# Performance work log

Hardware: AMD Instinct MI355X
Metric: run time of the kernel (lower is better)

## Reference

```python
import jax, jax.numpy as jnp
import numpy as np

N_HEAD = 16
D_MODEL = 1024
D_K = D_MODEL // N_HEAD  # 64
LN_EPS = 1e-5


def setup_inputs() -> dict:
    key = jax.random.key(0)
    ks = jax.random.split(key, 12)
    B, L, D = 4, 2048, D_MODEL
    std_qkv = float(np.sqrt(2.0 / (D + D_K)))
    q = jax.random.normal(ks[0], (B, L, D), jnp.float32)
    k = jax.random.normal(ks[1], (B, L, D), jnp.float32)
    v = jax.random.normal(ks[2], (B, L, D), jnp.float32)
    Wq = jax.random.normal(ks[3], (D, D), jnp.float32) * std_qkv
    Wk = jax.random.normal(ks[4], (D, D), jnp.float32) * std_qkv
    Wv = jax.random.normal(ks[5], (D, D), jnp.float32) * std_qkv
    bq = jnp.zeros((D,), jnp.float32)
    bk = jnp.zeros((D,), jnp.float32)
    bv = jnp.zeros((D,), jnp.float32)
    # xavier normal for fc: std = sqrt(2/(fan_in+fan_out))
    Wo = jax.random.normal(ks[6], (D, D), jnp.float32) * float(np.sqrt(2.0 / (D + D)))
    bo = jnp.zeros((D,), jnp.float32)
    gamma = jnp.ones((D,), jnp.float32)
    beta = jnp.zeros((D,), jnp.float32)
    return {"q": q, "k": k, "v": v, "Wq": Wq, "bq": bq, "Wk": Wk, "bk": bk,
            "Wv": Wv, "bv": bv, "Wo": Wo, "bo": bo, "gamma": gamma, "beta": beta}


def _layer_norm(x, gamma, beta):
    mu = jnp.mean(x, axis=-1, keepdims=True)
    var = jnp.mean(jnp.square(x - mu), axis=-1, keepdims=True)
    return (x - mu) * jax.lax.rsqrt(var + LN_EPS) * gamma + beta


def reference(q, k, v, Wq, bq, Wk, bk, Wv, bv, Wo, bo, gamma, beta):
    B, Lq, D = q.shape
    Lk = k.shape[1]
    h, dk = N_HEAD, D_K
    residual = q
    # projections (torch Linear: x @ W.T + b), split heads -> (h, b, l, dk)
    qh = (q @ Wq.T + bq).reshape(B, Lq, h, dk).transpose(2, 0, 1, 3)
    kh = (k @ Wk.T + bk).reshape(B, Lk, h, dk).transpose(2, 0, 1, 3)
    vh = (v @ Wv.T + bv).reshape(B, Lk, h, dk).transpose(2, 0, 1, 3)
    temp = jnp.asarray(np.power(dk, 0.5), qh.dtype)
    scores = jnp.einsum('hbqd,hbkd->hbqk', qh, kh) / temp
    attn = jax.nn.softmax(scores, axis=-1)  # softmax over key dim (dim=2 of bmm view)
    out = jnp.einsum('hbqk,hbkd->hbqd', attn, vh)
    # (h,b,lq,dk) -> (b,lq,h*dk)
    out = out.transpose(1, 2, 0, 3).reshape(B, Lq, D)
    out = out @ Wo.T + bo  # dropout p=0.0 -> identity
    out = _layer_norm(out + residual, gamma, beta)
    attn_flat = attn.reshape(h * B, Lq, Lk)  # matches torch (n_head*sz_b, lq, lk)
    return out, attn_flat
```

## Files before the change

kernel.cpp:

```cpp
#include <hip/hip_runtime.h>
#include <stdint.h>

typedef short bf16x8 __attribute__((ext_vector_type(8)));
typedef float f32x4 __attribute__((ext_vector_type(4)));
typedef unsigned short us4 __attribute__((ext_vector_type(4)));
typedef unsigned short us8 __attribute__((ext_vector_type(8)));
typedef unsigned uint2v __attribute__((ext_vector_type(2)));

#define SCL 0.18033688011112042f

__device__ __forceinline__ unsigned short f2bf(float f) {
  union { float f; unsigned u; } v; v.f = f;
  unsigned r = v.u + 0x7fffu + ((v.u >> 16) & 1u);
  return (unsigned short)(r >> 16);
}

__device__ __forceinline__ unsigned cvtpk(float lo, float hi) {
  unsigned r;
  asm("v_cvt_pk_bf16_f32 %0, %1, %2" : "=v"(r) : "v"(lo), "v"(hi));
  return r;
}

__device__ __forceinline__ float bf2f(unsigned short h) {
  union { unsigned u; float f; } v; v.u = ((unsigned)h) << 16; return v.f;
}

#define GL2LDS(g, l) __builtin_amdgcn_global_load_lds( \
    (const __attribute__((address_space(1))) void*)(g), \
    (__attribute__((address_space(3))) void*)(l), 16, 0, 0)

__global__ __launch_bounds__(256) void convert_all(
    const float* __restrict__ q, const float* __restrict__ k, const float* __restrict__ v,
    const float* __restrict__ wq, const float* __restrict__ wk, const float* __restrict__ wv,
    const float* __restrict__ wo,
    unsigned short* __restrict__ qb, unsigned short* __restrict__ kb, unsigned short* __restrict__ vb,
    unsigned short* __restrict__ wqb, unsigned short* __restrict__ wkb, unsigned short* __restrict__ wvb,
    unsigned short* __restrict__ wob)
{
  const long NB = 8388608, NW = 1048576;
  long i = ((long)blockIdx.x * 256 + threadIdx.x) * 4;
  if (i >= 3*NB + 4*NW) return;
  const float* src; unsigned short* dst; long off;
  if (i < NB)              { src = q;  dst = qb;  off = i; }
  else if (i < 2*NB)       { src = k;  dst = kb;  off = i - NB; }
  else if (i < 3*NB)       { src = v;  dst = vb;  off = i - 2*NB; }
  else if (i < 3*NB+NW)    { src = wq; dst = wqb; off = i - 3*NB; }
  else if (i < 3*NB+2*NW)  { src = wk; dst = wkb; off = i - 3*NB - NW; }
  else if (i < 3*NB+3*NW)  { src = wv; dst = wvb; off = i - 3*NB - 2*NW; }
  else                     { src = wo; dst = wob; off = i - 3*NB - 3*NW; }
  float4 x = *(const float4*)(src + off);
  us4 o; o.x = f2bf(x.x); o.y = f2bf(x.y); o.z = f2bf(x.z); o.w = f2bf(x.w);
  *(us4*)(dst + off) = o;
}

__global__ __launch_bounds__(256, 2) void qkv_gemm(
    const unsigned short* __restrict__ qb, const unsigned short* __restrict__ kb,
    const unsigned short* __restrict__ vb,
    const unsigned short* __restrict__ wqb, const unsigned short* __restrict__ wkb,
    const unsigned short* __restrict__ wvb,
    const float* __restrict__ bq, const float* __restrict__ bk, const float* __restrict__ bv,
    unsigned short* __restrict__ qh, unsigned short* __restrict__ kh,
    unsigned short* __restrict__ vt)
{
  const int z = blockIdx.z;
  const unsigned short* X = (z == 0) ? qb : (z == 1) ? kb : vb;
  const unsigned short* W = (z == 0) ? wqb : (z == 1) ? wkb : wvb;
  const float* bias = (z == 0) ? bq : (z == 1) ? bk : bv;
  unsigned short* dqh = (z == 0) ? qh : kh;
  const float sc = (z == 0) ? SCL : 1.0f;

  const int flat = blockIdx.x + (blockIdx.y << 6);
  const int xcd = flat & 7, ii = flat >> 3;
  const int m0 = (xcd * 8 + (ii & 7)) * 128;
  const int n0 = (ii >> 3) * 128;

  const int tid = threadIdx.x, lane = tid & 63, w = tid >> 6;
  const int wr = w >> 1, wc = w & 1;
  const int lg = lane >> 4, ll = lane & 15;

  __shared__ __align__(16) unsigned short As[2 * 128 * 32];
  __shared__ __align__(16) unsigned short Bs[2 * 128 * 32];

  f32x4 acc[4][4] = {};

  const char* gA = (const char*)X + ((size_t)(m0 + w*32 + (lane >> 2)) * 1024) * 2 + (lane & 3) * 16;
  const char* gB = (const char*)W + ((size_t)(n0 + w*32 + (lane >> 2)) * 1024) * 2 + (lane & 3) * 16;

#define STAGE_G(buf) do { \
    char* lA_ = (char*)As + (buf)*8192 + w*2048; \
    char* lB_ = (char*)Bs + (buf)*8192 + w*2048; \
    GL2LDS(gA, lA_); GL2LDS(gA + 32768, lA_ + 1024); \
    GL2LDS(gB, lB_); GL2LDS(gB + 32768, lB_ + 1024); \
    gA += 64; gB += 64; } while (0)

  STAGE_G(0);
  __syncthreads();

  for (int k0 = 0; k0 < 1024; k0 += 32) {
    const int cur = (k0 >> 5) & 1;
    if (k0 < 992) STAGE_G(cur ^ 1);
    const unsigned short* Ac = As + cur * 4096;
    const unsigned short* Bc = Bs + cur * 4096;
    bf16x8 xa[4], wb[4];
    const int kc = lg * 8;
#pragma unroll
    for (int f = 0; f < 4; ++f) xa[f] = *(const bf16x8*)&Ac[(wr*64 + f*16 + ll)*32 + kc];
#pragma unroll
    for (int f = 0; f < 4; ++f) wb[f] = *(const bf16x8*)&Bc[(wc*64 + f*16 + ll)*32 + kc];
    if (z < 2) {
#pragma unroll
      for (int fn = 0; fn < 4; ++fn)
#pragma unroll
        for (int fm = 0; fm < 4; ++fm)
          acc[fn][fm] = __builtin_amdgcn_mfma_f32_16x16x32_bf16(wb[fn], xa[fm], acc[fn][fm], 0, 0, 0);
    } else {
#pragma unroll
      for (int fm = 0; fm < 4; ++fm)
#pragma unroll
        for (int fn = 0; fn < 4; ++fn)
          acc[fm][fn] = __builtin_amdgcn_mfma_f32_16x16x32_bf16(xa[fm], wb[fn], acc[fm][fn], 0, 0, 0);
    }
    __syncthreads();
  }

  if (z < 2) {
#pragma unroll
    for (int fn = 0; fn < 4; ++fn) {
      const int n_g = n0 + wc*64 + fn*16 + lg*4;
      const float4 b4 = *(const float4*)&bias[n_g];
      const int h = n_g >> 6, dkk = n_g & 63;
#pragma unroll
      for (int fm = 0; fm < 4; ++fm) {
        const int m_g = m0 + wr*64 + fm*16 + ll;
        const int b_ = m_g >> 11, l_ = m_g & 2047;
        us4 pk;
        pk.x = f2bf((acc[fn][fm][0] + b4.x) * sc);
        pk.y = f2bf((acc[fn][fm][1] + b4.y) * sc);
        pk.z = f2bf((acc[fn][fm][2] + b4.z) * sc);
        pk.w = f2bf((acc[fn][fm][3] + b4.w) * sc);
        *(us4*)&dqh[((size_t)(h*4 + b_) * 2048 + l_) * 64 + dkk] = pk;
      }
    }
  } else {
#pragma unroll
    for (int fn = 0; fn < 4; ++fn) {
      const int n_g = n0 + wc*64 + fn*16 + ll;
      const float bias_n = bias[n_g];
      const int h = n_g >> 6, dkk = n_g & 63;
#pragma unroll
      for (int fm = 0; fm < 4; ++fm) {
        const int mrow = m0 + wr*64 + fm*16 + lg*4;
        const int b_ = mrow >> 11, l_ = mrow & 2047;
        us4 pk;
        pk.x = f2bf(acc[fm][fn][0] + bias_n);
        pk.y = f2bf(acc[fm][fn][1] + bias_n);
        pk.z = f2bf(acc[fm][fn][2] + bias_n);
        pk.w = f2bf(acc[fm][fn][3] + bias_n);
        *(us4*)&vt[((size_t)(h*4 + b_) * 64 + dkk) * 2048 + l_] = pk;
      }
    }
  }
}

__global__ __launch_bounds__(256, 3) void attn_kernel(
    const unsigned short* __restrict__ qh, const unsigned short* __restrict__ kh,
    const unsigned short* __restrict__ vt, float* __restrict__ probs,
    unsigned short* __restrict__ attn_o)
{
  const int bid = blockIdx.x;
  const int xcd = bid & 7;
  const int idx = bid >> 3;
  const int hb  = xcd * 8 + (idx & 7);
  const int qt  = idx >> 3;

  const int tid = threadIdx.x, lane = tid & 63, w = tid >> 6;
  const int wr = w >> 1, wc = w & 1;
  const int lg = lane >> 4, ll = lane & 15;

  __shared__ __align__(16) char smem[38400];
  unsigned short* Pb = (unsigned short*)smem;
  float* rs   = (float*)(smem + 36864);
  float* invl = (float*)(smem + 37888);
  float* Ored = (float*)smem;

  const size_t slab = (size_t)hb << 17;

  bf16x8 qf[4][2];
#pragma unroll
  for (int fq = 0; fq < 4; ++fq)
#pragma unroll
    for (int dh = 0; dh < 2; ++dh)
      qf[fq][dh] = *(const bf16x8*)&qh[slab + (size_t)(qt*128 + wr*64 + fq*16 + ll)*64 + dh*32 + lg*8];

  const unsigned short* Kf = kh + slab + (size_t)(wc*32 + ll)*64 + lg*8;
  const unsigned short* Vf = vt + slab + (size_t)ll*2048 + wc*32 + lg*8;

  float rsum[4] = {0.f, 0.f, 0.f, 0.f};
  for (int kt = 0; kt < 32; ++kt) {
    bf16x8 ka[2][2];
#pragma unroll
    for (int fk = 0; fk < 2; ++fk)
#pragma unroll
      for (int dh = 0; dh < 2; ++dh)
        ka[fk][dh] = *(const bf16x8*)(Kf + kt*4096 + fk*1024 + dh*32);
    f32x4 s[2][4] = {};
    __builtin_amdgcn_s_setprio(1);
#pragma unroll
    for (int dh = 0; dh < 2; ++dh)
#pragma unroll
      for (int fk = 0; fk < 2; ++fk)
#pragma unroll
        for (int fq = 0; fq < 4; ++fq)
          s[fk][fq] = __builtin_amdgcn_mfma_f32_16x16x32_bf16(ka[fk][dh], qf[fq][dh], s[fk][fq], 0, 0, 0);
    __builtin_amdgcn_s_setprio(0);
#pragma unroll
    for (int fk = 0; fk < 2; ++fk)
#pragma unroll
      for (int fq = 0; fq < 4; ++fq)
#pragma unroll
        for (int r = 0; r < 4; ++r)
          rsum[fq] += exp2f(s[fk][fq][r]);
  }

#pragma unroll
  for (int fq = 0; fq < 4; ++fq) {
    float t = rsum[fq];
    t += __shfl_xor(t, 16);
    t += __shfl_xor(t, 32);
    rsum[fq] = t;
  }
  if (lg == 0) {
#pragma unroll
    for (int fq = 0; fq < 4; ++fq)
      rs[wc*128 + wr*64 + fq*16 + ll] = rsum[fq];
  }
  __syncthreads();
  if (tid < 128) invl[tid] = 1.0f / (rs[tid] + rs[128 + tid]);
  __syncthreads();
  float inv_r[4];
#pragma unroll
  for (int fq = 0; fq < 4; ++fq) inv_r[fq] = invl[wr*64 + fq*16 + ll];

  f32x4 o[4][4] = {};
  float* pb2 = probs + ((size_t)hb << 22) + (size_t)(qt*128) * 2048;
  const int prow = tid >> 4, pcol = (tid & 15) * 4;

  for (int kt = 0; kt < 32; ++kt) {
    unsigned short* Pc = Pb + (kt & 1) * 9216;
    bf16x8 vb[4];
#pragma unroll
    for (int f = 0; f < 4; ++f)
      vb[f] = *(const bf16x8*)(Vf + f*32768 + kt*64);

    bf16x8 ka[2][2];
#pragma unroll
    for (int fk = 0; fk < 2; ++fk)
#pragma unroll
      for (int dh = 0; dh < 2; ++dh)
        ka[fk][dh] = *(const bf16x8*)(Kf + kt*4096 + fk*1024 + dh*32);

    f32x4 s[2][4] = {};
    __builtin_amdgcn_s_setprio(1);
#pragma unroll
    for (int dh = 0; dh < 2; ++dh)
#pragma unroll
      for (int fk = 0; fk < 2; ++fk)
#pragma unroll
        for (int fq = 0; fq < 4; ++fq)
          s[fk][fq] = __builtin_amdgcn_mfma_f32_16x16x32_bf16(ka[fk][dh], qf[fq][dh], s[fk][fq], 0, 0, 0);
    __builtin_amdgcn_s_setprio(0);

#pragma unroll
    for (int fk = 0; fk < 2; ++fk)
#pragma unroll
      for (int fq = 0; fq < 4; ++fq) {
        float p0 = exp2f(s[fk][fq][0]) * inv_r[fq];
        float p1 = exp2f(s[fk][fq][1]) * inv_r[fq];
        float p2 = exp2f(s[fk][fq][2]) * inv_r[fq];
        float p3 = exp2f(s[fk][fq][3]) * inv_r[fq];
        uint2v u; u.x = cvtpk(p0, p1); u.y = cvtpk(p2, p3);
        *(uint2v*)&Pc[(wr*64 + fq*16 + ll)*72 + wc*32 + fk*16 + lg*4] = u;
      }
    __syncthreads();

    bf16x8 pa[4];
#pragma unroll
    for (int fm = 0; fm < 4; ++fm)
      pa[fm] = *(const bf16x8*)&Pc[(wr*64 + fm*16 + ll)*72 + wc*32 + lg*8];
    __builtin_amdgcn_s_setprio(1);
#pragma unroll
    for (int fm = 0; fm < 4; ++fm)
#pragma unroll
      for (int fd = 0; fd < 4; ++fd)
        o[fm][fd] = __builtin_amdgcn_mfma_f32_16x16x32_bf16(pa[fm], vb[fd], o[fm][fd], 0, 0, 0);
    __builtin_amdgcn_s_setprio(0);

    float* pdst = pb2 + kt*64;
#pragma unroll
    for (int j = 0; j < 8; ++j) {
      const int row = j*16 + prow;
      us4 pv = *(const us4*)&Pc[row*72 + pcol];
      f32x4 pf; pf[0] = bf2f(pv.x); pf[1] = bf2f(pv.y); pf[2] = bf2f(pv.z); pf[3] = bf2f(pv.w);
      __builtin_nontemporal_store(pf, (f32x4*)(pdst + (size_t)row*2048 + pcol));
    }
  }

  __syncthreads();
  if (wc == 1) {
#pragma unroll
    for (int fm = 0; fm < 4; ++fm)
#pragma unroll
      for (int fd = 0; fd < 4; ++fd)
#pragma unroll
        for (int r = 0; r < 4; ++r)
          Ored[wr*4096 + (fm*16 + lg*4 + r)*64 + fd*16 + ll] = o[fm][fd][r];
  }
  __syncthreads();
  if (wc == 0) {
    const int b_ = hb & 3, h = hb >> 2;
#pragma unroll
    for (int fm = 0; fm < 4; ++fm)
#pragma unroll
      for (int fd = 0; fd < 4; ++fd)
#pragma unroll
        for (int r = 0; r < 4; ++r) {
          const int qrow = fm*16 + lg*4 + r;
          const int d = fd*16 + ll;
          float val = o[fm][fd][r] + Ored[wr*4096 + qrow*64 + d];
          const int mg = b_*2048 + qt*128 + wr*64 + qrow;
          attn_o[(size_t)mg*1024 + h*64 + d] = f2bf(val);
        }
  }
}

__global__ __launch_bounds__(256, 2) void outproj_gemm(
    const unsigned short* __restrict__ Ain, const unsigned short* __restrict__ Wob,
    const float* __restrict__ bo, const float* __restrict__ qres, float* __restrict__ preLN)
{
  const int flat = blockIdx.x + (blockIdx.y << 6);
  const int xcd = flat & 7, ii = flat >> 3;
  const int m0 = (xcd * 8 + (ii & 7)) * 128;
  const int n0 = (ii >> 3) * 128;

  const int tid = threadIdx.x, lane = tid & 63, w = tid >> 6;
  const int wr = w >> 1, wc = w & 1;
  const int lg = lane >> 4, ll = lane & 15;

  __shared__ __align__(16) unsigned short As[2 * 128 * 32];
  __shared__ __align__(16) unsigned short Bs[2 * 128 * 32];

  f32x4 acc[4][4] = {};

  const char* gA = (const char*)Ain + ((size_t)(m0 + w*32 + (lane >> 2)) * 1024) * 2 + (lane & 3) * 16;
  const char* gB = (const char*)Wob + ((size_t)(n0 + w*32 + (lane >> 2)) * 1024) * 2 + (lane & 3) * 16;

  STAGE_G(0);
  __syncthreads();

  for (int k0 = 0; k0 < 1024; k0 += 32) {
    const int cur = (k0 >> 5) & 1;
    if (k0 < 992) STAGE_G(cur ^ 1);
    const unsigned short* Ac = As + cur * 4096;
    const unsigned short* Bc = Bs + cur * 4096;
    bf16x8 xa[4], wb[4];
    const int kc = lg * 8;
#pragma unroll
    for (int f = 0; f < 4; ++f) xa[f] = *(const bf16x8*)&Ac[(wr*64 + f*16 + ll)*32 + kc];
#pragma unroll
    for (int f = 0; f < 4; ++f) wb[f] = *(const bf16x8*)&Bc[(wc*64 + f*16 + ll)*32 + kc];
#pragma unroll
    for (int fn = 0; fn < 4; ++fn)
#pragma unroll
      for (int fm = 0; fm < 4; ++fm)
        acc[fn][fm] = __builtin_amdgcn_mfma_f32_16x16x32_bf16(wb[fn], xa[fm], acc[fn][fm], 0, 0, 0);
    __syncthreads();
  }

#pragma unroll
  for (int fn = 0; fn < 4; ++fn) {
    const int n_g = n0 + wc*64 + fn*16 + lg*4;
    const float4 b4 = *(const float4*)&bo[n_g];
#pragma unroll
    for (int fm = 0; fm < 4; ++fm) {
      const int m_g = m0 + wr*64 + fm*16 + ll;
      const size_t idxp = (size_t)m_g * 1024 + n_g;
      const float4 r4 = *(const float4*)&qres[idxp];
      f32x4 y;
      y[0] = acc[fn][fm][0] + b4.x + r4.x;
      y[1] = acc[fn][fm][1] + b4.y + r4.y;
      y[2] = acc[fn][fm][2] + b4.z + r4.z;
      y[3] = acc[fn][fm][3] + b4.w + r4.w;
      *(f32x4*)&preLN[idxp] = y;
    }
  }
}

__global__ __launch_bounds__(256) void ln_kernel(
    const float* __restrict__ x, const float* __restrict__ gamma,
    const float* __restrict__ beta, float* __restrict__ out)
{
  const int row = blockIdx.x, tid = threadIdx.x;
  const float4 xv = ((const float4*)(x + (size_t)row * 1024))[tid];
  float s = xv.x + xv.y + xv.z + xv.w;
  float ss = xv.x*xv.x + xv.y*xv.y + xv.z*xv.z + xv.w*xv.w;
#pragma unroll
  for (int m = 1; m < 64; m <<= 1) { s += __shfl_xor(s, m); ss += __shfl_xor(ss, m); }
  __shared__ float red[8];
  if ((tid & 63) == 0) { red[(tid >> 6)*2] = s; red[(tid >> 6)*2 + 1] = ss; }
  __syncthreads();
  s  = red[0] + red[2] + red[4] + red[6];
  ss = red[1] + red[3] + red[5] + red[7];
  const float mu = s * (1.0f/1024.0f);
  const float var = ss * (1.0f/1024.0f) - mu*mu;
  const float rstd = rsqrtf(var + 1e-5f);
  const float4 g  = ((const float4*)gamma)[tid];
  const float4 be = ((const float4*)beta)[tid];
  float4 y;
  y.x = (xv.x - mu)*rstd*g.x + be.x;
  y.y = (xv.y - mu)*rstd*g.y + be.y;
  y.z = (xv.z - mu)*rstd*g.z + be.z;
  y.w = (xv.w - mu)*rstd*g.w + be.w;
  ((float4*)(out + (size_t)row * 1024))[tid] = y;
}

extern "C" void kernel_launch(void* const* d_in, const int* in_sizes, int n_in,
                              void* d_out, int out_size, void* d_ws, size_t ws_size,
                              hipStream_t stream) {
  const float* q     = (const float*)d_in[0];
  const float* k     = (const float*)d_in[1];
  const float* v     = (const float*)d_in[2];
  const float* Wq    = (const float*)d_in[3];
  const float* bq    = (const float*)d_in[4];
  const float* Wk    = (const float*)d_in[5];
  const float* bk    = (const float*)d_in[6];
  const float* Wv    = (const float*)d_in[7];
  const float* bv    = (const float*)d_in[8];
  const float* Wo    = (const float*)d_in[9];
  const float* bo    = (const float*)d_in[10];
  const float* gamma = (const float*)d_in[11];
  const float* beta  = (const float*)d_in[12];

  float* out   = (float*)d_out;
  float* probs = out + 8388608;

  char* ws = (char*)d_ws;
  unsigned short* qb  = (unsigned short*)(ws);
  unsigned short* kb  = (unsigned short*)(ws + 16777216);
  unsigned short* vb  = (unsigned short*)(ws + 33554432);
  unsigned short* wqb = (unsigned short*)(ws + 50331648);
  unsigned short* wkb = (unsigned short*)(ws + 52428800);
  unsigned short* wvb = (unsigned short*)(ws + 54525952);
  unsigned short* wob = (unsigned short*)(ws + 56623104);
  unsigned short* qh  = (unsigned short*)(ws + 58720256);
  unsigned short* kh  = (unsigned short*)(ws + 75497472);
  unsigned short* vt  = (unsigned short*)(ws + 92274688);
  float* preLN = (float*)(ws);
  unsigned short* attn_o = vb;

  convert_all<<<28672, 256, 0, stream>>>(q, k, v, Wq, Wk, Wv, Wo,
                                         qb, kb, vb, wqb, wkb, wvb, wob);

  dim3 g1(64, 8, 3);
  qkv_gemm<<<g1, 256, 0, stream>>>(qb, kb, vb, wqb, wkb, wvb, bq, bk, bv, qh, kh, vt);

  attn_kernel<<<1024, 256, 0, stream>>>(qh, kh, vt, probs, attn_o);

  dim3 g3(64, 8);
  outproj_gemm<<<g3, 256, 0, stream>>>(attn_o, wob, bo, q, preLN);

  ln_kernel<<<8192, 256, 0, stream>>>(preLN, gamma, beta, out);
}
```

Before: 544.3 us.

## Process two query tiles per attention block, fusing tile B row-sum into tile A pass

Each attention block now handles two 128-row query tiles. The second tile's softmax row-sum pass runs inside the first tile's probability/PV loop and shares the same K fragment loads, which removes one full separate K sweep per pair of tiles. The grid is halved to 512 blocks and launch bounds drop to 2 waves per SIMD to make room for the extra Q fragments and accumulators. The cost is more register pressure, lower occupancy, and a longer serial path per block.

New measurement: 456.7 us. 1.19x faster.

```diff
diff --git a/kernel.cpp b/kernel.cpp
--- a/kernel.cpp
+++ b/kernel.cpp
@@ -162,7 +162,7 @@
   }
 }
 
-__global__ __launch_bounds__(256, 3) void attn_kernel(
+__global__ __launch_bounds__(256, 2) void attn_kernel(
     const unsigned short* __restrict__ qh, const unsigned short* __restrict__ kh,
     const unsigned short* __restrict__ vt, float* __restrict__ probs,
     unsigned short* __restrict__ attn_o)
@@ -171,7 +171,8 @@
   const int xcd = bid & 7;
   const int idx = bid >> 3;
   const int hb  = xcd * 8 + (idx & 7);
-  const int qt  = idx >> 3;
+  const int qp  = idx >> 3;
+  const int qt_a = qp * 2, qt_b = qp * 2 + 1;
 
   const int tid = threadIdx.x, lane = tid & 63, w = tid >> 6;
   const int wr = w >> 1, wc = w & 1;
@@ -185,15 +186,19 @@
 
   const size_t slab = (size_t)hb << 17;
 
-  bf16x8 qf[4][2];
+  bf16x8 qfa[4][2], qfb[4][2];
 #pragma unroll
   for (int fq = 0; fq < 4; ++fq)
 #pragma unroll
-    for (int dh = 0; dh < 2; ++dh)
-      qf[fq][dh] = *(const bf16x8*)&qh[slab + (size_t)(qt*128 + wr*64 + fq*16 + ll)*64 + dh*32 + lg*8];
+    for (int dh = 0; dh < 2; ++dh) {
+      qfa[fq][dh] = *(const bf16x8*)&qh[slab + (size_t)(qt_a*128 + wr*64 + fq*16 + ll)*64 + dh*32 + lg*8];
+      qfb[fq][dh] = *(const bf16x8*)&qh[slab + (size_t)(qt_b*128 + wr*64 + fq*16 + ll)*64 + dh*32 + lg*8];
+    }
 
   const unsigned short* Kf = kh + slab + (size_t)(wc*32 + ll)*64 + lg*8;
   const unsigned short* Vf = vt + slab + (size_t)ll*2048 + wc*32 + lg*8;
+
+  const int prow = tid >> 4, pcol = (tid & 15) * 4;
 
   float rsum[4] = {0.f, 0.f, 0.f, 0.f};
   for (int kt = 0; kt < 32; ++kt) {
@@ -211,7 +216,7 @@
       for (int fk = 0; fk < 2; ++fk)
 #pragma unroll
         for (int fq = 0; fq < 4; ++fq)
-          s[fk][fq] = __builtin_amdgcn_mfma_f32_16x16x32_bf16(ka[fk][dh], qf[fq][dh], s[fk][fq], 0, 0, 0);
+          s[fk][fq] = __builtin_amdgcn_mfma_f32_16x16x32_bf16(ka[fk][dh], qfa[fq][dh], s[fk][fq], 0, 0, 0);
     __builtin_amdgcn_s_setprio(0);
 #pragma unroll
     for (int fk = 0; fk < 2; ++fk)
@@ -237,13 +242,14 @@
   __syncthreads();
   if (tid < 128) invl[tid] = 1.0f / (rs[tid] + rs[128 + tid]);
   __syncthreads();
-  float inv_r[4];
-#pragma unroll
-  for (int fq = 0; fq < 4; ++fq) inv_r[fq] = invl[wr*64 + fq*16 + ll];
+  float inv_ra[4];
+#pragma unroll
+  for (int fq = 0; fq < 4; ++fq) inv_ra[fq] = invl[wr*64 + fq*16 + ll];
+  __syncthreads();
 
   f32x4 o[4][4] = {};
-  float* pb2 = probs + ((size_t)hb << 22) + (size_t)(qt*128) * 2048;
-  const int prow = tid >> 4, pcol = (tid & 15) * 4;
+  float rsb[4] = {0.f, 0.f, 0.f, 0.f};
+  float* pb2a = probs + ((size_t)hb << 22) + (size_t)(qt_a*128) * 2048;
 
   for (int kt = 0; kt < 32; ++kt) {
     unsigned short* Pc = Pb + (kt & 1) * 9216;
@@ -251,7 +257,6 @@
 #pragma unroll
     for (int f = 0; f < 4; ++f)
       vb[f] = *(const bf16x8*)(Vf + f*32768 + kt*64);
-
     bf16x8 ka[2][2];
 #pragma unroll
     for (int fk = 0; fk < 2; ++fk)
@@ -259,6 +264,26 @@
       for (int dh = 0; dh < 2; ++dh)
         ka[fk][dh] = *(const bf16x8*)(Kf + kt*4096 + fk*1024 + dh*32);
 
+    {
+      f32x4 sb[2][4] = {};
+      __builtin_amdgcn_s_setprio(1);
+#pragma unroll
+      for (int dh = 0; dh < 2; ++dh)
+#pragma unroll
+        for (int fk = 0; fk < 2; ++fk)
+#pragma unroll
+          for (int fq = 0; fq < 4; ++fq)
+            sb[fk][fq] = __builtin_amdgcn_mfma_f32_16x16x32_bf16(ka[fk][dh], qfb[fq][dh], sb[fk][fq], 0, 0, 0);
+      __builtin_amdgcn_s_setprio(0);
+#pragma unroll
+      for (int fk = 0; fk < 2; ++fk)
+#pragma unroll
+        for (int fq = 0; fq < 4; ++fq)
+#pragma unroll
+          for (int r = 0; r < 4; ++r)
+            rsb[fq] += exp2f(sb[fk][fq][r]);
+    }
+
     f32x4 s[2][4] = {};
     __builtin_amdgcn_s_setprio(1);
 #pragma unroll
@@ -267,17 +292,16 @@
       for (int fk = 0; fk < 2; ++fk)
 #pragma unroll
         for (int fq = 0; fq < 4; ++fq)
-          s[fk][fq] = __builtin_amdgcn_mfma_f32_16x16x32_bf16(ka[fk][dh], qf[fq][dh], s[fk][fq], 0, 0, 0);
+          s[fk][fq] = __builtin_amdgcn_mfma_f32_16x16x32_bf16(ka[fk][dh], qfa[fq][dh], s[fk][fq], 0, 0, 0);
     __builtin_amdgcn_s_setprio(0);
-
 #pragma unroll
     for (int fk = 0; fk < 2; ++fk)
 #pragma unroll
       for (int fq = 0; fq < 4; ++fq) {
-        float p0 = exp2f(s[fk][fq][0]) * inv_r[fq];
-        float p1 = exp2f(s[fk][fq][1]) * inv_r[fq];
-        float p2 = exp2f(s[fk][fq][2]) * inv_r[fq];
-        float p3 = exp2f(s[fk][fq][3]) * inv_r[fq];
+        float p0 = exp2f(s[fk][fq][0]) * inv_ra[fq];
+        float p1 = exp2f(s[fk][fq][1]) * inv_ra[fq];
+        float p2 = exp2f(s[fk][fq][2]) * inv_ra[fq];
+        float p3 = exp2f(s[fk][fq][3]) * inv_ra[fq];
         uint2v u; u.x = cvtpk(p0, p1); u.y = cvtpk(p2, p3);
         *(uint2v*)&Pc[(wr*64 + fq*16 + ll)*72 + wc*32 + fk*16 + lg*4] = u;
       }
@@ -295,7 +319,7 @@
         o[fm][fd] = __builtin_amdgcn_mfma_f32_16x16x32_bf16(pa[fm], vb[fd], o[fm][fd], 0, 0, 0);
     __builtin_amdgcn_s_setprio(0);
 
-    float* pdst = pb2 + kt*64;
+    float* pdst = pb2a + kt*64;
 #pragma unroll
     for (int j = 0; j < 8; ++j) {
       const int row = j*16 + prow;
@@ -306,6 +330,18 @@
   }
 
   __syncthreads();
+#pragma unroll
+  for (int fq = 0; fq < 4; ++fq) {
+    float t = rsb[fq];
+    t += __shfl_xor(t, 16);
+    t += __shfl_xor(t, 32);
+    rsb[fq] = t;
+  }
+  if (lg == 0) {
+#pragma unroll
+    for (int fq = 0; fq < 4; ++fq)
+      rs[wc*128 + wr*64 + fq*16 + ll] = rsb[fq];
+  }
   if (wc == 1) {
 #pragma unroll
     for (int fm = 0; fm < 4; ++fm)
@@ -316,6 +352,7 @@
           Ored[wr*4096 + (fm*16 + lg*4 + r)*64 + fd*16 + ll] = o[fm][fd][r];
   }
   __syncthreads();
+  if (tid < 128) invl[tid] = 1.0f / (rs[tid] + rs[128 + tid]);
   if (wc == 0) {
     const int b_ = hb & 3, h = hb >> 2;
 #pragma unroll
@@ -327,7 +364,105 @@
           const int qrow = fm*16 + lg*4 + r;
           const int d = fd*16 + ll;
           float val = o[fm][fd][r] + Ored[wr*4096 + qrow*64 + d];
-          const int mg = b_*2048 + qt*128 + wr*64 + qrow;
+          const int mg = b_*2048 + qt_a*128 + wr*64 + qrow;
+          attn_o[(size_t)mg*1024 + h*64 + d] = f2bf(val);
+        }
+  }
+  __syncthreads();
+  float inv_rb[4];
+#pragma unroll
+  for (int fq = 0; fq < 4; ++fq) inv_rb[fq] = invl[wr*64 + fq*16 + ll];
+  __syncthreads();
+
+#pragma unroll
+  for (int fm = 0; fm < 4; ++fm)
+#pragma unroll
+    for (int fd = 0; fd < 4; ++fd)
+      o[fm][fd] = f32x4{0.f, 0.f, 0.f, 0.f};
+  float* pb2b = probs + ((size_t)hb << 22) + (size_t)(qt_b*128) * 2048;
+
+  for (int kt = 0; kt < 32; ++kt) {
+    unsigned short* Pc = Pb + (kt & 1) * 9216;
+    bf16x8 vb[4];
+#pragma unroll
+    for (int f = 0; f < 4; ++f)
+      vb[f] = *(const bf16x8*)(Vf + f*32768 + kt*64);
+    bf16x8 ka[2][2];
+#pragma unroll
+    for (int fk = 0; fk < 2; ++fk)
+#pragma unroll
+      for (int dh = 0; dh < 2; ++dh)
+        ka[fk][dh] = *(const bf16x8*)(Kf + kt*4096 + fk*1024 + dh*32);
+
+    f32x4 s[2][4] = {};
+    __builtin_amdgcn_s_setprio(1);
+#pragma unroll
+    for (int dh = 0; dh < 2; ++dh)
+#pragma unroll
+      for (int fk = 0; fk < 2; ++fk)
+#pragma unroll
+        for (int fq = 0; fq < 4; ++fq)
+          s[fk][fq] = __builtin_amdgcn_mfma_f32_16x16x32_bf16(ka[fk][dh], qfb[fq][dh], s[fk][fq], 0, 0, 0);
+    __builtin_amdgcn_s_setprio(0);
+
+#pragma unroll
+    for (int fk = 0; fk < 2; ++fk)
+#pragma unroll
+      for (int fq = 0; fq < 4; ++fq) {
+        float p0 = exp2f(s[fk][fq][0]) * inv_rb[fq];
+        float p1 = exp2f(s[fk][fq][1]) * inv_rb[fq];
+        float p2 = exp2f(s[fk][fq][2]) * inv_rb[fq];
+        float p3 = exp2f(s[fk][fq][3]) * inv_rb[fq];
+        uint2v u; u.x = cvtpk(p0, p1); u.y = cvtpk(p2, p3);
+        *(uint2v*)&Pc[(wr*64 + fq*16 + ll)*72 + wc*32 + fk*16 + lg*4] = u;
+      }
+    __syncthreads();
+
+    bf16x8 pa[4];
+#pragma unroll
+    for (int fm = 0; fm < 4; ++fm)
+      pa[fm] = *(const bf16x8*)&Pc[(wr*64 + fm*16 + ll)*72 + wc*32 + lg*8];
+    __builtin_amdgcn_s_setprio(1);
+#pragma unroll
+    for (int fm = 0; fm < 4; ++fm)
+#pragma unroll
+      for (int fd = 0; fd < 4; ++fd)
+        o[fm][fd] = __builtin_amdgcn_mfma_f32_16x16x32_bf16(pa[fm], vb[fd], o[fm][fd], 0, 0, 0);
+    __builtin_amdgcn_s_setprio(0);
+
+    float* pdst = pb2b + kt*64;
+#pragma unroll
+    for (int j = 0; j < 8; ++j) {
+      const int row = j*16 + prow;
+      us4 pv = *(const us4*)&Pc[row*72 + pcol];
+      f32x4 pf; pf[0] = bf2f(pv.x); pf[1] = bf2f(pv.y); pf[2] = bf2f(pv.z); pf[3] = bf2f(pv.w);
+      __builtin_nontemporal_store(pf, (f32x4*)(pdst + (size_t)row*2048 + pcol));
+    }
+  }
+
+  __syncthreads();
+  if (wc == 1) {
+#pragma unroll
+    for (int fm = 0; fm < 4; ++fm)
+#pragma unroll
+      for (int fd = 0; fd < 4; ++fd)
+#pragma unroll
+        for (int r = 0; r < 4; ++r)
+          Ored[wr*4096 + (fm*16 + lg*4 + r)*64 + fd*16 + ll] = o[fm][fd][r];
+  }
+  __syncthreads();
+  if (wc == 0) {
+    const int b_ = hb & 3, h = hb >> 2;
+#pragma unroll
+    for (int fm = 0; fm < 4; ++fm)
+#pragma unroll
+      for (int fd = 0; fd < 4; ++fd)
+#pragma unroll
+        for (int r = 0; r < 4; ++r) {
+          const int qrow = fm*16 + lg*4 + r;
+          const int d = fd*16 + ll;
+          float val = o[fm][fd][r] + Ored[wr*4096 + qrow*64 + d];
+          const int mg = b_*2048 + qt_b*128 + wr*64 + qrow;
           attn_o[(size_t)mg*1024 + h*64 + d] = f2bf(val);
         }
   }
@@ -463,7 +598,7 @@
   dim3 g1(64, 8, 3);
   qkv_gemm<<<g1, 256, 0, stream>>>(qb, kb, vb, wqb, wkb, wvb, bq, bk, bv, qh, kh, vt);
 
-  attn_kernel<<<1024, 256, 0, stream>>>(qh, kh, vt, probs, attn_o);
+  attn_kernel<<<512, 256, 0, stream>>>(qh, kh, vt, probs, attn_o);
 
   dim3 g3(64, 8);
   outproj_gemm<<<g3, 256, 0, stream>>>(attn_o, wob, bo, q, preLN);
```
